# Kernel tuning notes

Hardware: AMD Instinct MI355X
Metric: run time of the kernel (lower is better)

## Reference

```python
import jax, jax.numpy as jnp
import numpy as np
import math

NUM_HEADS = 16
THETA = 10000.0


def _rope(x, token_pos, theta):
    # x: [B, H, S, d_k]; token_pos: [S]
    d_k = x.shape[-1]
    freqs = 1.0 / theta ** (jnp.arange(0, d_k, 2, dtype=jnp.float32) / d_k)  # [d_k/2]
    angles = token_pos.astype(jnp.float32)[:, None] * freqs[None, :]         # [S, d_k/2]
    cos, sin = jnp.cos(angles), jnp.sin(angles)
    x1 = x[..., 0::2]
    x2 = x[..., 1::2]
    out1 = x1 * cos - x2 * sin
    out2 = x1 * sin + x2 * cos
    # interleave back: (..., d_k/2, 2) -> (..., d_k)
    return jnp.stack([out1, out2], axis=-1).reshape(x.shape)


def setup_inputs() -> dict:
    key = jax.random.key(0)
    ks = jax.random.split(key, 5)
    B, S, D = 4, 2048, 1024
    scale = 0.02
    return {
        "x": jax.random.normal(ks[0], (B, S, D), dtype=jnp.float32),
        "token_pos": jnp.arange(S, dtype=jnp.int64 if jax.config.jax_enable_x64 else jnp.int32),
        "Wq": jax.random.normal(ks[1], (D, D), dtype=jnp.float32) * scale,
        "Wk": jax.random.normal(ks[2], (D, D), dtype=jnp.float32) * scale,
        "Wv": jax.random.normal(ks[3], (D, D), dtype=jnp.float32) * scale,
        "Wo": jax.random.normal(ks[4], (D, D), dtype=jnp.float32) * scale,
    }


def reference(x, token_pos, Wq, Wk, Wv, Wo):
    B, S, D = x.shape
    H = NUM_HEADS
    d_k = D // H
    # projections (Linear without bias: y = x @ W^T, W is [out, in])
    def proj(W):
        y = jnp.einsum('bsd,ed->bse', x, W)
        return y.reshape(B, S, H, d_k).transpose(0, 2, 1, 3)  # [B,H,S,d_k]
    q, k, v = proj(Wq), proj(Wk), proj(Wv)
    q = _rope(q, token_pos, THETA)
    k = _rope(k, token_pos, THETA)
    scores = jnp.einsum('bhqd,bhkd->bhqk', q, k) / math.sqrt(d_k)
    causal = jnp.tril(jnp.ones((S, S), dtype=bool))
    scores = jnp.where(causal, scores, -jnp.inf)
    attn = jax.nn.softmax(scores, axis=-1)
    out = jnp.einsum('bhqk,bhkd->bhqd', attn, v)            # [B,H,S,d_k]
    out = out.transpose(0, 2, 1, 3).reshape(B, S, D)
    return jnp.einsum('bsd,ed->bse', out, Wo)
```

## Files before the change

kernel.cpp:

```cpp
#include <hip/hip_runtime.h>

typedef unsigned short u16;
typedef __bf16 bf16x8 __attribute__((ext_vector_type(8)));
typedef float f32x4 __attribute__((ext_vector_type(4)));
typedef u16 u16x8 __attribute__((ext_vector_type(8)));

#define B_ 4
#define S_ 2048
#define D_ 1024
#define H_ 16
#define LOG2E 1.44269504f

__device__ inline u16 f2bf(float f) {
  unsigned u = __float_as_uint(f);
  u = u + 0x7fffu + ((u >> 16) & 1u);
  return (u16)(u >> 16);
}
__device__ inline u16 f2bf_hw(float f) {
  __bf16 b = (__bf16)f;
  return __builtin_bit_cast(u16, b);
}
__device__ inline float bf2f(u16 h) {
  return __uint_as_float(((unsigned)h) << 16);
}
__device__ inline void gload_lds16(const u16* g, u16* l) {
  __builtin_amdgcn_global_load_lds((const __attribute__((address_space(1))) void*)g,
                                   (__attribute__((address_space(3))) void*)l, 16, 0, 0);
}
__device__ inline float fast_exp2(float x) {
  float r;
  asm("v_exp_f32 %0, %1" : "=v"(r) : "v"(x));
  return r;
}

__global__ __launch_bounds__(256) void k_prep(const float* __restrict__ x,
                                              const float* __restrict__ w0,
                                              const float* __restrict__ w1,
                                              const float* __restrict__ w2,
                                              const float* __restrict__ w3,
                                              const int* __restrict__ pos,
                                              u16* __restrict__ xb,
                                              u16* __restrict__ wdst,
                                              float2* __restrict__ tab) {
  const int bid = blockIdx.x;
  if (bid < 8192) {
    int i = bid * 256 + threadIdx.x;
    float4 v = reinterpret_cast<const float4*>(x)[i];
    ushort4 o;
    o.x = f2bf(v.x); o.y = f2bf(v.y); o.z = f2bf(v.z); o.w = f2bf(v.w);
    reinterpret_cast<ushort4*>(xb)[i] = o;
  } else if (bid < 12288) {
    int i = (bid - 8192) * 256 + threadIdx.x;
    const int tensor = i >> 18;
    const int local = i & 262143;
    const float* s = tensor == 0 ? w0 : tensor == 1 ? w1 : tensor == 2 ? w2 : w3;
    float4 v = reinterpret_cast<const float4*>(s)[local];
    ushort4 o;
    o.x = f2bf(v.x); o.y = f2bf(v.y); o.z = f2bf(v.z); o.w = f2bf(v.w);
    reinterpret_cast<ushort4*>(wdst + (size_t)tensor * 1048576)[local] = o;
  } else {
    int idx = (bid - 12288) * 256 + threadIdx.x;
    int s = idx >> 5, i = idx & 31;
    float freq = powf(10000.0f, -(float)i * (1.0f / 32.0f));
    float ang = (float)pos[s] * freq;
    float sn, c;
    sincosf(ang, &sn, &c);
    tab[idx] = make_float2(c, sn);
  }
}

__global__ __launch_bounds__(256) void k_rope_k(u16* __restrict__ kb,
                                                const float2* __restrict__ tab) {
  int idx = blockIdx.x * 256 + threadIdx.x;
  const int row = idx >> 7;
  const int s = row & 2047;
  const int chunk = idx & 127;
  u16* p = kb + ((size_t)row << 10) + chunk * 8;
  u16x8 v = *reinterpret_cast<u16x8*>(p);
  const float4* tp = reinterpret_cast<const float4*>(tab + s * 32 + (chunk & 7) * 4);
  float4 t0 = tp[0], t1 = tp[1];
  float cc[4] = {t0.x, t0.z, t1.x, t1.z};
  float ss[4] = {t0.y, t0.w, t1.y, t1.w};
  u16x8 o;
#pragma unroll
  for (int u = 0; u < 4; u++) {
    float x1 = bf2f(v[2 * u]), x2 = bf2f(v[2 * u + 1]);
    o[2 * u]     = f2bf(x1 * cc[u] - x2 * ss[u]);
    o[2 * u + 1] = f2bf(x1 * ss[u] + x2 * cc[u]);
  }
  *reinterpret_cast<u16x8*>(p) = o;
}

__global__ __launch_bounds__(512) void k_gemm_qk(const u16* __restrict__ A,
                                                 const u16* __restrict__ Bqk,
                                                 u16* __restrict__ Cqk) {
  __shared__ u16 As[2][256 * 64];
  __shared__ u16 Bs[2][256 * 64];
  const int K = 1024;
  const int xcd = blockIdx.x & 7;
  const int idx = blockIdx.x >> 3;
  const int by = xcd * 4 + (idx & 3);
  const int bx = idx >> 2;
  const int m0 = by << 8, n0 = bx << 8;
  const int tid = threadIdx.x;
  const int lane = tid & 63, w = tid >> 6;
  const int wr = w >> 2, wc = w & 3;
  const int r = lane & 15, g = lane >> 4;

  f32x4 acc[8][4] = {};

  const int srow = tid >> 3;
  const int scol = (((tid & 7) ^ ((tid >> 3) & 7)) * 8);
  const int csw = r & 7;

  const u16* Ab = A + (size_t)(m0 + srow) * K + scol;
  const u16* Bb = Bqk + (size_t)(n0 + srow) * K + scol;

#define STG(k0v, bf) do {                                                \
    gload_lds16(Ab + (k0v),                   &As[bf][0] + tid * 8);     \
    gload_lds16(Ab + (k0v) + (size_t)64 * K,  &As[bf][0] + tid * 8 + 4096);  \
    gload_lds16(Ab + (k0v) + (size_t)128 * K, &As[bf][0] + tid * 8 + 8192);  \
    gload_lds16(Ab + (k0v) + (size_t)192 * K, &As[bf][0] + tid * 8 + 12288); \
    gload_lds16(Bb + (k0v),                   &Bs[bf][0] + tid * 8);     \
    gload_lds16(Bb + (k0v) + (size_t)64 * K,  &Bs[bf][0] + tid * 8 + 4096);  \
    gload_lds16(Bb + (k0v) + (size_t)128 * K, &Bs[bf][0] + tid * 8 + 8192);  \
    gload_lds16(Bb + (k0v) + (size_t)192 * K, &Bs[bf][0] + tid * 8 + 12288); \
  } while (0)

  STG(0, 0);

  for (int t = 0; t < 16; ++t) {
    const int bsel = t & 1;
    if (t < 15) {
      STG((t + 1) * 64, bsel ^ 1);
      asm volatile("s_waitcnt vmcnt(8)" ::: "memory");
    } else {
      asm volatile("s_waitcnt vmcnt(0)" ::: "memory");
    }
    __builtin_amdgcn_s_barrier();
    asm volatile("" ::: "memory");

    const u16* Ah = &As[bsel][(wr * 128) * 64];
    const u16* Bh = &Bs[bsel][(wc * 64) * 64];
#pragma unroll
    for (int ks = 0; ks < 2; ks++) {
      bf16x8 bfr[4];
#pragma unroll
      for (int t2 = 0; t2 < 4; t2++)
        bfr[t2] = *reinterpret_cast<const bf16x8*>(
            &Bh[(t2 * 16 + r) * 64 + (((ks * 4 + g) ^ csw) * 8)]);
#pragma unroll
      for (int i = 0; i < 8; i++) {
        bf16x8 af = *reinterpret_cast<const bf16x8*>(
            &Ah[(i * 16 + r) * 64 + (((ks * 4 + g) ^ csw) * 8)]);
#pragma unroll
        for (int t2 = 0; t2 < 4; t2++)
          acc[i][t2] = __builtin_amdgcn_mfma_f32_16x16x32_bf16(af, bfr[t2], acc[i][t2], 0, 0, 0);
      }
    }
    asm volatile("" ::: "memory");
    __builtin_amdgcn_s_barrier();
  }
#undef STG

  u16* Cb = Cqk + (size_t)(n0 >> 10) * (8192 * 1024);
  const int c0 = n0 & 1023;
#pragma unroll
  for (int i = 0; i < 8; i++) {
#pragma unroll
    for (int t2 = 0; t2 < 4; t2++) {
      const int row = m0 + wr * 128 + i * 16 + g * 4;
      const int col = c0 + wc * 64 + t2 * 16 + r;
#pragma unroll
      for (int j = 0; j < 4; j++)
        Cb[(size_t)(row + j) * 1024 + col] = f2bf(acc[i][t2][j]);
    }
  }
}

__global__ __launch_bounds__(256) void k_gemm_v(const u16* __restrict__ A,
                                                const u16* __restrict__ Bw,
                                                u16* __restrict__ Vt) {
  __shared__ u16 As[2][128 * 64];
  __shared__ u16 Bs[2][128 * 64];
  const int K = 1024;
  const int xcd = blockIdx.x & 7;
  const int idx = blockIdx.x >> 3;
  const int by = xcd * 8 + (idx & 7);
  const int bx = idx >> 3;
  const int m0 = by << 7, n0 = bx << 7;
  const int tid = threadIdx.x;
  const int lane = tid & 63;
  const int wv = tid >> 6;
  const int wm = (wv >> 1) << 6;
  const int wn = (wv & 1) << 6;
  const int r = lane & 15, g = lane >> 4;

  f32x4 acc[4][4] = {};

  const int srow0 = tid >> 3;
  const int scol = (((tid & 7) ^ ((tid >> 3) & 7)) * 8);
  const int csw = r & 7;

  const u16* Ab = A + (size_t)(m0 + srow0) * K + scol;
  const u16* Bb = Bw + (size_t)(n0 + srow0) * K + scol;

#define STAGEV(k0v, bf) do {                                       \
    const u16* a_ = Ab + (k0v);                                    \
    const u16* b_ = Bb + (k0v);                                    \
    gload_lds16(a_,                &As[bf][0] + tid * 8);          \
    gload_lds16(a_ + (size_t)32 * K, &As[bf][0] + tid * 8 + 2048); \
    gload_lds16(a_ + (size_t)64 * K, &As[bf][0] + tid * 8 + 4096); \
    gload_lds16(a_ + (size_t)96 * K, &As[bf][0] + tid * 8 + 6144); \
    gload_lds16(b_,                &Bs[bf][0] + tid * 8);          \
    gload_lds16(b_ + (size_t)32 * K, &Bs[bf][0] + tid * 8 + 2048); \
    gload_lds16(b_ + (size_t)64 * K, &Bs[bf][0] + tid * 8 + 4096); \
    gload_lds16(b_ + (size_t)96 * K, &Bs[bf][0] + tid * 8 + 6144); \
  } while (0)

  STAGEV(0, 0);

  for (int t = 0; t < 16; ++t) {
    const int bsel = t & 1;
    if (t < 15) {
      STAGEV((t + 1) * 64, bsel ^ 1);
      asm volatile("s_waitcnt vmcnt(8)" ::: "memory");
    } else {
      asm volatile("s_waitcnt vmcnt(0)" ::: "memory");
    }
    __builtin_amdgcn_s_barrier();
    asm volatile("" ::: "memory");

#pragma unroll
    for (int ks = 0; ks < 2; ks++) {
      bf16x8 af[4], bfr[4];
#pragma unroll
      for (int i = 0; i < 4; i++)
        af[i] = *reinterpret_cast<const bf16x8*>(
            &As[bsel][(wm + i * 16 + r) * 64 + (((ks * 4 + g) ^ csw) * 8)]);
#pragma unroll
      for (int t2 = 0; t2 < 4; t2++)
        bfr[t2] = *reinterpret_cast<const bf16x8*>(
            &Bs[bsel][(wn + t2 * 16 + r) * 64 + (((ks * 4 + g) ^ csw) * 8)]);
#pragma unroll
      for (int i = 0; i < 4; i++)
#pragma unroll
        for (int t2 = 0; t2 < 4; t2++)
          acc[i][t2] = __builtin_amdgcn_mfma_f32_16x16x32_bf16(af[i], bfr[t2], acc[i][t2], 0, 0, 0);
    }
    asm volatile("" ::: "memory");
    __builtin_amdgcn_s_barrier();
  }
#undef STAGEV

#pragma unroll
  for (int i = 0; i < 4; i++) {
#pragma unroll
    for (int t = 0; t < 4; t++) {
      const int row = m0 + wm + i * 16 + g * 4;
      const int col = n0 + wn + t * 16 + r;
      const int b = row >> 11, s0 = row & 2047;
      const int h = col >> 6, d = col & 63;
      ushort4 o;
      o.x = f2bf(acc[i][t][0]); o.y = f2bf(acc[i][t][1]);
      o.z = f2bf(acc[i][t][2]); o.w = f2bf(acc[i][t][3]);
      *reinterpret_cast<ushort4*>(
          Vt + (((size_t)(b * 16 + h) * 64 + d) << 11) + s0) = o;
    }
  }
}

__global__ __launch_bounds__(256) void k_gemm_bt(const u16* __restrict__ A,
                                                 const u16* __restrict__ Bw,
                                                 float* __restrict__ C,
                                                 int M, int N, int K) {
  __shared__ u16 As[2][128 * 64];
  __shared__ u16 Bs[2][128 * 64];
  const int nbx = N >> 7;
  const int swz = (blockIdx.x & 7) * (gridDim.x >> 3) + (blockIdx.x >> 3);
  const int bx = swz % nbx;
  const int by = swz / nbx;
  const int m0 = by << 7, n0 = bx << 7;
  const int tid = threadIdx.x;
  const int lane = tid & 63;
  const int wv = tid >> 6;
  const int wm = (wv >> 1) << 6;
  const int wn = (wv & 1) << 6;
  const int r = lane & 15, g = lane >> 4;

  f32x4 acc[4][4] = {};

  const int srow0 = tid >> 3;
  const int scol = (((tid & 7) ^ ((tid >> 3) & 7)) * 8);
  const int csw = r & 7;

  const u16* Ab = A + (size_t)(m0 + srow0) * K + scol;
  const u16* Bb = Bw + (size_t)(n0 + srow0) * K + scol;
  const int nt = K >> 6;

#define STAGEW(k0v, bf) do {                                       \
    const u16* a_ = Ab + (k0v);                                    \
    const u16* b_ = Bb + (k0v);                                    \
    gload_lds16(a_,                &As[bf][0] + tid * 8);          \
    gload_lds16(a_ + (size_t)32 * K, &As[bf][0] + tid * 8 + 2048); \
    gload_lds16(a_ + (size_t)64 * K, &As[bf][0] + tid * 8 + 4096); \
    gload_lds16(a_ + (size_t)96 * K, &As[bf][0] + tid * 8 + 6144); \
    gload_lds16(b_,                &Bs[bf][0] + tid * 8);          \
    gload_lds16(b_ + (size_t)32 * K, &Bs[bf][0] + tid * 8 + 2048); \
    gload_lds16(b_ + (size_t)64 * K, &Bs[bf][0] + tid * 8 + 4096); \
    gload_lds16(b_ + (size_t)96 * K, &Bs[bf][0] + tid * 8 + 6144); \
  } while (0)

  STAGEW(0, 0);

  for (int t = 0; t < nt; ++t) {
    const int bsel = t & 1;
    if (t < nt - 1) {
      STAGEW((t + 1) * 64, bsel ^ 1);
      asm volatile("s_waitcnt vmcnt(8)" ::: "memory");
    } else {
      asm volatile("s_waitcnt vmcnt(0)" ::: "memory");
    }
    __builtin_amdgcn_s_barrier();
    asm volatile("" ::: "memory");

#pragma unroll
    for (int ks = 0; ks < 2; ks++) {
      bf16x8 af[4], bfr[4];
#pragma unroll
      for (int i = 0; i < 4; i++)
        af[i] = *reinterpret_cast<const bf16x8*>(
            &As[bsel][(wm + i * 16 + r) * 64 + (((ks * 4 + g) ^ csw) * 8)]);
#pragma unroll
      for (int t2 = 0; t2 < 4; t2++)
        bfr[t2] = *reinterpret_cast<const bf16x8*>(
            &Bs[bsel][(wn + t2 * 16 + r) * 64 + (((ks * 4 + g) ^ csw) * 8)]);
#pragma unroll
      for (int i = 0; i < 4; i++)
#pragma unroll
        for (int t2 = 0; t2 < 4; t2++)
          acc[i][t2] = __builtin_amdgcn_mfma_f32_16x16x32_bf16(af[i], bfr[t2], acc[i][t2], 0, 0, 0);
    }
    asm volatile("" ::: "memory");
    __builtin_amdgcn_s_barrier();
  }
#undef STAGEW

#pragma unroll
  for (int i = 0; i < 4; i++) {
#pragma unroll
    for (int t = 0; t < 4; t++) {
      const int row = m0 + wm + i * 16 + g * 4;
      const int col = n0 + wn + t * 16 + r;
#pragma unroll
      for (int j = 0; j < 4; j++)
        C[(size_t)(row + j) * N + col] = acc[i][t][j];
    }
  }
}

__global__ __launch_bounds__(256) void k_attn14(const u16* __restrict__ Q,
                                                const u16* __restrict__ Kb,
                                                const u16* __restrict__ Vt,
                                                const float2* __restrict__ tab,
                                                u16* __restrict__ O) {
  __shared__ u16 Ks[64 * 64];
  __shared__ u16 Vs[64 * 64];
  __shared__ u16 Ps[4][32 * 64];

  const int bh = (blockIdx.x & 7) * 8 + ((blockIdx.x >> 3) & 7);
  const int qt = 15 - (blockIdx.x >> 6);
  const int b = bh >> 4, h = bh & 15;
  const int tid = threadIdx.x;
  const int lane = tid & 63, w = tid >> 6;
  const int g = lane >> 4, r = lane & 15;

  const u16* Kbase = Kb + (size_t)(b * S_) * 1024 + h * 64;
  const u16* Vbase = Vt + (size_t)bh * 64 * 2048;

  const int srow = tid >> 3;
  const int scol = ((tid & 7) * 8) ^ ((srow & 7) * 8);
  const int rsw = (r & 7) * 8;

  const int qbase = qt << 7;
  const int qrow0 = qbase + (w << 5);

  const float QSC = 0.125f * LOG2E;
  bf16x8 qf[2][2];
#pragma unroll
  for (int f = 0; f < 2; f++) {
    const int s = qrow0 + f * 16 + r;
    const u16* qrow = Q + (size_t)(b * S_ + s) * 1024 + h * 64;
    qf[f][0] = *reinterpret_cast<const bf16x8*>(qrow + g * 8);
    qf[f][1] = *reinterpret_cast<const bf16x8*>(qrow + 32 + g * 8);
    const float4* tp = reinterpret_cast<const float4*>(tab + s * 32);
#pragma unroll
    for (int c = 0; c < 2; c++) {
      float4 t0 = tp[c * 8 + g * 2], t1 = tp[c * 8 + g * 2 + 1];
      float cc[4] = {t0.x, t0.z, t1.x, t1.z};
      float ss[4] = {t0.y, t0.w, t1.y, t1.w};
      bf16x8 q = qf[f][c];
#pragma unroll
      for (int u = 0; u < 4; u++) {
        float x1 = (float)q[2 * u], x2 = (float)q[2 * u + 1];
        q[2 * u]     = (__bf16)((x1 * cc[u] - x2 * ss[u]) * QSC);
        q[2 * u + 1] = (__bf16)((x1 * ss[u] + x2 * cc[u]) * QSC);
      }
      qf[f][c] = q;
    }
  }

  bf16x8 ones;
#pragma unroll
  for (int u = 0; u < 8; u++) ones[u] = (__bf16)1.0f;

  f32x4 o_acc[2][4] = {};
  f32x4 lacc[2] = {};
  u16* pb0 = &Ps[w][r * 64];
  u16* pb1 = &Ps[w][(16 + r) * 64];

  const u16* kp0 = Kbase + (size_t)srow * 1024 + scol;
  const u16* kp1 = kp0 + 32 * 1024;
  const u16* vp0 = Vbase + (size_t)srow * 2048 + scol;
  const u16* vp1 = vp0 + 32 * 2048;

  const int kend = qbase + 128;
  for (int k0 = 0; k0 < kend; k0 += 64) {
    gload_lds16(kp0, Ks + tid * 8);
    gload_lds16(kp1, Ks + tid * 8 + 2048);
    gload_lds16(vp0, Vs + tid * 8);
    gload_lds16(vp1, Vs + tid * 8 + 2048);
    kp0 += 64 * 1024; kp1 += 64 * 1024; vp0 += 64; vp1 += 64;
    __syncthreads();

    if (k0 <= qrow0 + 31) {
      const int rem0 = qrow0 + 15 - k0;
      const int rem1 = qrow0 + 31 - k0;
      const int ktlim0 = rem0 < 0 ? 0 : (rem0 >= 48 ? 4 : (rem0 >> 4) + 1);
      const int ktlim1 = rem1 >= 48 ? 4 : (rem1 >> 4) + 1;
      const bool mask0 = (k0 + 63 > qrow0);
      const bool mask1 = (k0 + 63 > qrow0 + 16);

#pragma unroll
      for (int kt = 0; kt < 4; kt++) {
        const int pc = (kt * 16 + g * 4) ^ rsw;
        if (kt >= ktlim1) {
          ushort4 z = {0, 0, 0, 0};
          *reinterpret_cast<ushort4*>(pb0 + pc) = z;
          *reinterpret_cast<ushort4*>(pb1 + pc) = z;
          continue;
        }
        const int krow = kt * 16 + r;
        bf16x8 kf0 = *reinterpret_cast<const bf16x8*>(&Ks[krow * 64 + ((g * 8) ^ rsw)]);
        bf16x8 kf1 = *reinterpret_cast<const bf16x8*>(&Ks[krow * 64 + ((32 + g * 8) ^ rsw)]);
        f32x4 s0 = {}, s1 = {};
        if (kt < ktlim0) {
          s0 = __builtin_amdgcn_mfma_f32_16x16x32_bf16(kf0, qf[0][0], s0, 0, 0, 0);
          s0 = __builtin_amdgcn_mfma_f32_16x16x32_bf16(kf1, qf[0][1], s0, 0, 0, 0);
        }
        s1 = __builtin_amdgcn_mfma_f32_16x16x32_bf16(kf0, qf[1][0], s1, 0, 0, 0);
        s1 = __builtin_amdgcn_mfma_f32_16x16x32_bf16(kf1, qf[1][1], s1, 0, 0, 0);

        const int colb = k0 + kt * 16 + g * 4;
        float p0[4], p1[4];
        if (kt < ktlim0) {
          if (mask0) {
#pragma unroll
            for (int j = 0; j < 4; j++)
              if (colb + j > qrow0 + r) s0[j] = -1e30f;
          }
#pragma unroll
          for (int j = 0; j < 4; j++) p0[j] = fast_exp2(s0[j]);
        } else {
#pragma unroll
          for (int j = 0; j < 4; j++) p0[j] = 0.f;
        }
        if (mask1) {
#pragma unroll
          for (int j = 0; j < 4; j++)
            if (colb + j > qrow0 + 16 + r) s1[j] = -1e30f;
        }
#pragma unroll
        for (int j = 0; j < 4; j++) p1[j] = fast_exp2(s1[j]);

        ushort4 w0, w1;
        w0.x = f2bf_hw(p0[0]); w0.y = f2bf_hw(p0[1]); w0.z = f2bf_hw(p0[2]); w0.w = f2bf_hw(p0[3]);
        w1.x = f2bf_hw(p1[0]); w1.y = f2bf_hw(p1[1]); w1.z = f2bf_hw(p1[2]); w1.w = f2bf_hw(p1[3]);
        *reinterpret_cast<ushort4*>(pb0 + pc) = w0;
        *reinterpret_cast<ushort4*>(pb1 + pc) = w1;
      }
      asm volatile("s_waitcnt lgkmcnt(0)" ::: "memory");

#pragma unroll
      for (int kc = 0; kc < 2; kc++) {
        const int cb = (kc * 32 + g * 8) ^ rsw;
        bf16x8 pf0 = *reinterpret_cast<const bf16x8*>(pb0 + cb);
        bf16x8 pf1 = *reinterpret_cast<const bf16x8*>(pb1 + cb);
        lacc[0] = __builtin_amdgcn_mfma_f32_16x16x32_bf16(pf0, ones, lacc[0], 0, 0, 0);
        lacc[1] = __builtin_amdgcn_mfma_f32_16x16x32_bf16(pf1, ones, lacc[1], 0, 0, 0);
#pragma unroll
        for (int dt = 0; dt < 4; dt++) {
          bf16x8 vf = *reinterpret_cast<const bf16x8*>(
              &Vs[(dt * 16 + r) * 64 + ((kc * 32 + g * 8) ^ rsw)]);
          o_acc[0][dt] = __builtin_amdgcn_mfma_f32_16x16x32_bf16(pf0, vf, o_acc[0][dt], 0, 0, 0);
          o_acc[1][dt] = __builtin_amdgcn_mfma_f32_16x16x32_bf16(pf1, vf, o_acc[1][dt], 0, 0, 0);
        }
      }
    }
    __syncthreads();
  }

#pragma unroll
  for (int f = 0; f < 2; f++) {
    u16* orow = O + (size_t)(b * S_ + qrow0 + f * 16) * 1024 + h * 64;
#pragma unroll
    for (int j = 0; j < 4; j++) {
      const float rln = 1.0f / lacc[f][j];
#pragma unroll
      for (int dt = 0; dt < 4; dt++)
        orow[(size_t)(g * 4 + j) * 1024 + dt * 16 + r] = f2bf(o_acc[f][dt][j] * rln);
    }
  }
}

extern "C" void kernel_launch(void* const* d_in, const int* in_sizes, int n_in,
                              void* d_out, int out_size, void* d_ws, size_t ws_size,
                              hipStream_t stream) {
  const float* x  = (const float*)d_in[0];
  const int*   pos = (const int*)d_in[1];
  const float* Wq = (const float*)d_in[2];
  const float* Wk = (const float*)d_in[3];
  const float* Wv = (const float*)d_in[4];
  const float* Wo = (const float*)d_in[5];
  float* out = (float*)d_out;

  char* ws = (char*)d_ws;
  size_t off = 0;
  auto alloc = [&](size_t bytes) {
    void* p = ws + off;
    off += (bytes + 255) & ~(size_t)255;
    return p;
  };
  const size_t XB = (size_t)8192 * 1024 * 2;
  u16* xb  = (u16*)alloc(XB);
  u16* wqb = (u16*)alloc((size_t)1024 * 1024 * 2);
  u16* wkb = (u16*)alloc((size_t)1024 * 1024 * 2);
  u16* wvb = (u16*)alloc((size_t)1024 * 1024 * 2);
  u16* wob = (u16*)alloc((size_t)1024 * 1024 * 2);
  u16* qb  = (u16*)alloc(XB);
  u16* kb  = (u16*)alloc(XB);
  u16* ob  = (u16*)alloc(XB);
  u16* vt  = (u16*)alloc(XB);
  float2* tab = (float2*)alloc((size_t)2048 * 32 * sizeof(float2));
  (void)wkb;

  k_prep<<<12544, 256, 0, stream>>>(x, Wq, Wk, Wv, Wo, pos, xb, wqb, tab);

  k_gemm_qk<<<256, 512, 0, stream>>>(xb, wqb, qb);

  k_gemm_v<<<512, 256, 0, stream>>>(xb, wvb, vt);

  k_rope_k<<<4096, 256, 0, stream>>>(kb, tab);

  k_attn14<<<1024, 256, 0, stream>>>(qb, kb, vt, tab, ob);

  k_gemm_bt<<<512, 256, 0, stream>>>(ob, wob, out, 8192, 1024, 1024);
}
```

Baseline: 167.2 us.

## Double-buffer K/V tiles in attention and halve per-wave P scratch

The attention kernel now double-buffers the K and V tiles in LDS. The next tile's global-to-LDS loads are issued before the current tile is computed, and partial vmcnt waits replace the full syncthreads, so memory latency is meant to overlap with MFMA work. The P scratch per wave is halved by writing the two 16-row halves one after the other through the same buffer, holding the second half in registers meanwhile. V fragments are loaded into registers once and reused by both halves. LDS use grows for K/V and register pressure rises, which may reduce occupancy.

```diff
diff --git a/kernel.cpp b/kernel.cpp
--- a/kernel.cpp
+++ b/kernel.cpp
@@ -359,14 +359,14 @@
   }
 }
 
-__global__ __launch_bounds__(256) void k_attn14(const u16* __restrict__ Q,
+__global__ __launch_bounds__(256) void k_attn15(const u16* __restrict__ Q,
                                                 const u16* __restrict__ Kb,
                                                 const u16* __restrict__ Vt,
                                                 const float2* __restrict__ tab,
                                                 u16* __restrict__ O) {
-  __shared__ u16 Ks[64 * 64];
-  __shared__ u16 Vs[64 * 64];
-  __shared__ u16 Ps[4][32 * 64];
+  __shared__ u16 Ks[2][64 * 64];
+  __shared__ u16 Vs[2][64 * 64];
+  __shared__ u16 Ps[4][16 * 64];
 
   const int bh = (blockIdx.x & 7) * 8 + ((blockIdx.x >> 3) & 7);
   const int qt = 15 - (blockIdx.x >> 6);
@@ -416,24 +416,40 @@
 
   f32x4 o_acc[2][4] = {};
   f32x4 lacc[2] = {};
-  u16* pb0 = &Ps[w][r * 64];
-  u16* pb1 = &Ps[w][(16 + r) * 64];
+  u16* pb = &Ps[w][r * 64];
 
   const u16* kp0 = Kbase + (size_t)srow * 1024 + scol;
   const u16* kp1 = kp0 + 32 * 1024;
   const u16* vp0 = Vbase + (size_t)srow * 2048 + scol;
   const u16* vp1 = vp0 + 32 * 2048;
 
-  const int kend = qbase + 128;
-  for (int k0 = 0; k0 < kend; k0 += 64) {
-    gload_lds16(kp0, Ks + tid * 8);
-    gload_lds16(kp1, Ks + tid * 8 + 2048);
-    gload_lds16(vp0, Vs + tid * 8);
-    gload_lds16(vp1, Vs + tid * 8 + 2048);
-    kp0 += 64 * 1024; kp1 += 64 * 1024; vp0 += 64; vp1 += 64;
-    __syncthreads();
+#define STAGE_KV(bf) do {                               \
+    gload_lds16(kp0, &Ks[bf][0] + tid * 8);             \
+    gload_lds16(kp1, &Ks[bf][0] + tid * 8 + 2048);      \
+    gload_lds16(vp0, &Vs[bf][0] + tid * 8);             \
+    gload_lds16(vp1, &Vs[bf][0] + tid * 8 + 2048);      \
+    kp0 += 64 * 1024; kp1 += 64 * 1024; vp0 += 64; vp1 += 64; \
+  } while (0)
+
+  const int nt = (qt << 1) + 2;
+
+  STAGE_KV(0);
+
+  for (int t = 0; t < nt; ++t) {
+    const int bsel = t & 1;
+    const int k0 = t << 6;
+    if (t < nt - 1) {
+      STAGE_KV(bsel ^ 1);
+      asm volatile("s_waitcnt vmcnt(4)" ::: "memory");
+    } else {
+      asm volatile("s_waitcnt vmcnt(0)" ::: "memory");
+    }
+    __builtin_amdgcn_s_barrier();
+    asm volatile("" ::: "memory");
 
     if (k0 <= qrow0 + 31) {
+      const u16* ks = &Ks[bsel][0];
+      const u16* vs = &Vs[bsel][0];
       const int rem0 = qrow0 + 15 - k0;
       const int rem1 = qrow0 + 31 - k0;
       const int ktlim0 = rem0 < 0 ? 0 : (rem0 >= 48 ? 4 : (rem0 >> 4) + 1);
@@ -441,18 +457,19 @@
       const bool mask0 = (k0 + 63 > qrow0);
       const bool mask1 = (k0 + 63 > qrow0 + 16);
 
+      ushort4 w1s[4];
 #pragma unroll
       for (int kt = 0; kt < 4; kt++) {
         const int pc = (kt * 16 + g * 4) ^ rsw;
         if (kt >= ktlim1) {
           ushort4 z = {0, 0, 0, 0};
-          *reinterpret_cast<ushort4*>(pb0 + pc) = z;
-          *reinterpret_cast<ushort4*>(pb1 + pc) = z;
+          *reinterpret_cast<ushort4*>(pb + pc) = z;
+          w1s[kt] = z;
           continue;
         }
         const int krow = kt * 16 + r;
-        bf16x8 kf0 = *reinterpret_cast<const bf16x8*>(&Ks[krow * 64 + ((g * 8) ^ rsw)]);
-        bf16x8 kf1 = *reinterpret_cast<const bf16x8*>(&Ks[krow * 64 + ((32 + g * 8) ^ rsw)]);
+        bf16x8 kf0 = *reinterpret_cast<const bf16x8*>(&ks[krow * 64 + ((g * 8) ^ rsw)]);
+        bf16x8 kf1 = *reinterpret_cast<const bf16x8*>(&ks[krow * 64 + ((32 + g * 8) ^ rsw)]);
         f32x4 s0 = {}, s1 = {};
         if (kt < ktlim0) {
           s0 = __builtin_amdgcn_mfma_f32_16x16x32_bf16(kf0, qf[0][0], s0, 0, 0, 0);
@@ -486,29 +503,50 @@
         ushort4 w0, w1;
         w0.x = f2bf_hw(p0[0]); w0.y = f2bf_hw(p0[1]); w0.z = f2bf_hw(p0[2]); w0.w = f2bf_hw(p0[3]);
         w1.x = f2bf_hw(p1[0]); w1.y = f2bf_hw(p1[1]); w1.z = f2bf_hw(p1[2]); w1.w = f2bf_hw(p1[3]);
-        *reinterpret_cast<ushort4*>(pb0 + pc) = w0;
-        *reinterpret_cast<ushort4*>(pb1 + pc) = w1;
+        *reinterpret_cast<ushort4*>(pb + pc) = w0;
+        w1s[kt] = w1;
       }
       asm volatile("s_waitcnt lgkmcnt(0)" ::: "memory");
 
+      bf16x8 vfr[2][4];
+#pragma unroll
+      for (int kc = 0; kc < 2; kc++)
+#pragma unroll
+        for (int dt = 0; dt < 4; dt++)
+          vfr[kc][dt] = *reinterpret_cast<const bf16x8*>(
+              &vs[(dt * 16 + r) * 64 + ((kc * 32 + g * 8) ^ rsw)]);
+
 #pragma unroll
       for (int kc = 0; kc < 2; kc++) {
         const int cb = (kc * 32 + g * 8) ^ rsw;
-        bf16x8 pf0 = *reinterpret_cast<const bf16x8*>(pb0 + cb);
-        bf16x8 pf1 = *reinterpret_cast<const bf16x8*>(pb1 + cb);
+        bf16x8 pf0 = *reinterpret_cast<const bf16x8*>(pb + cb);
         lacc[0] = __builtin_amdgcn_mfma_f32_16x16x32_bf16(pf0, ones, lacc[0], 0, 0, 0);
+#pragma unroll
+        for (int dt = 0; dt < 4; dt++)
+          o_acc[0][dt] = __builtin_amdgcn_mfma_f32_16x16x32_bf16(pf0, vfr[kc][dt], o_acc[0][dt], 0, 0, 0);
+      }
+
+#pragma unroll
+      for (int kt = 0; kt < 4; kt++) {
+        const int pc = (kt * 16 + g * 4) ^ rsw;
+        *reinterpret_cast<ushort4*>(pb + pc) = w1s[kt];
+      }
+      asm volatile("s_waitcnt lgkmcnt(0)" ::: "memory");
+
+#pragma unroll
+      for (int kc = 0; kc < 2; kc++) {
+        const int cb = (kc * 32 + g * 8) ^ rsw;
+        bf16x8 pf1 = *reinterpret_cast<const bf16x8*>(pb + cb);
         lacc[1] = __builtin_amdgcn_mfma_f32_16x16x32_bf16(pf1, ones, lacc[1], 0, 0, 0);
 #pragma unroll
-        for (int dt = 0; dt < 4; dt++) {
-          bf16x8 vf = *reinterpret_cast<const bf16x8*>(
-              &Vs[(dt * 16 + r) * 64 + ((kc * 32 + g * 8) ^ rsw)]);
-          o_acc[0][dt] = __builtin_amdgcn_mfma_f32_16x16x32_bf16(pf0, vf, o_acc[0][dt], 0, 0, 0);
-          o_acc[1][dt] = __builtin_amdgcn_mfma_f32_16x16x32_bf16(pf1, vf, o_acc[1][dt], 0, 0, 0);
-        }
+        for (int dt = 0; dt < 4; dt++)
+          o_acc[1][dt] = __builtin_amdgcn_mfma_f32_16x16x32_bf16(pf1, vfr[kc][dt], o_acc[1][dt], 0, 0, 0);
       }
     }
-    __syncthreads();
-  }
+    asm volatile("" ::: "memory");
+    __builtin_amdgcn_s_barrier();
+  }
+#undef STAGE_KV
 
 #pragma unroll
   for (int f = 0; f < 2; f++) {
@@ -562,7 +600,7 @@
 
   k_rope_k<<<4096, 256, 0, stream>>>(kb, tab);
 
-  k_attn14<<<1024, 256, 0, stream>>>(qb, kb, vt, tab, ob);
+  k_attn15<<<1024, 256, 0, stream>>>(qb, kb, vt, tab, ob);
 
   k_gemm_bt<<<512, 256, 0, stream>>>(ob, wob, out, 8192, 1024, 1024);
 }
```

Measured after the change: 180.9 us. 8.2% more time.
